# Performance work log

Hardware: AMD Instinct MI355X
Metric: run time of the kernel (lower is better)

Reference implementation:

```python
import jax, jax.numpy as jnp
import numpy as np

N_NODES = 50000
N_EDGES = 400000
D_NODE = 256
D_EDGE = 64
LN_EPS = 1e-6  # flax LayerNorm default


def _layer_norm(x, scale, bias):
    mu = jnp.mean(x, axis=-1, keepdims=True)
    var = jnp.mean(jnp.square(x - mu), axis=-1, keepdims=True)
    return (x - mu) * jax.lax.rsqrt(var + LN_EPS) * scale + bias


def _glorot(key, shape):
    fan_in, fan_out = shape
    std = jnp.sqrt(2.0 / (fan_in + fan_out))
    return std * jax.random.normal(key, shape, dtype=jnp.float32)


def setup_inputs() -> dict:
    key = jax.random.key(0)
    ks = jax.random.split(key, 10)
    inp = {
        "nodes": jax.random.normal(ks[0], (N_NODES, D_NODE), dtype=jnp.float32),
        "edges": jax.random.normal(ks[1], (N_EDGES, D_EDGE), dtype=jnp.float32),
        "senders": jax.random.randint(ks[2], (N_EDGES,), 0, N_NODES, dtype=jnp.int32),
        "receivers": jax.random.randint(ks[3], (N_EDGES,), 0, N_NODES, dtype=jnp.int32),
        # message projection (no bias)
        "W_message": _glorot(ks[4], (D_NODE + D_EDGE, D_NODE)),
        # NodeMLP (ReluMLP_skip) with n_features_list_nodes = [256, 256, 256]
        "mlp_W0": _glorot(ks[5], (D_NODE, D_NODE)), "mlp_b0": jnp.zeros((D_NODE,), jnp.float32),
        "mlp_W1": _glorot(ks[6], (D_NODE, D_NODE)), "mlp_b1": jnp.zeros((D_NODE,), jnp.float32),
        "mlp_W2": _glorot(ks[7], (D_NODE, D_NODE)), "mlp_b2": jnp.zeros((D_NODE,), jnp.float32),
        # LayerNorm params
        "ln_aggr_scale": jnp.ones((D_NODE,), jnp.float32), "ln_aggr_bias": jnp.zeros((D_NODE,), jnp.float32),
        "ln_out_scale": jnp.ones((D_NODE,), jnp.float32), "ln_out_bias": jnp.zeros((D_NODE,), jnp.float32),
    }
    return inp


def _relu_mlp_skip(x, Ws, bs):
    # Dense layers; ReLU on all but the last; residual add whenever widths match.
    n = len(Ws)
    for i, (W, b) in enumerate(zip(Ws, bs)):
        y = x @ W + b
        if i < n - 1:
            y = jax.nn.relu(y)
        x = x + y if y.shape[-1] == x.shape[-1] else y
    return x


def reference(nodes, edges, senders, receivers, W_message,
              mlp_W0, mlp_b0, mlp_W1, mlp_b1, mlp_W2, mlp_b2,
              ln_aggr_scale, ln_aggr_bias, ln_out_scale, ln_out_bias):
    total_nodes = nodes.shape[0]
    sender_features = nodes[senders]                      # [E, d] gather
    msg_in = jnp.concatenate([sender_features, edges], axis=-1)  # [E, d+d_e]
    messages = msg_in @ W_message                          # [E, d]
    agg = jax.ops.segment_sum(messages, receivers, num_segments=total_nodes)  # [N, d]
    h = _layer_norm(jax.nn.relu(agg) + nodes, ln_aggr_scale, ln_aggr_bias)
    nodes_out = _relu_mlp_skip(h, [mlp_W0, mlp_W1, mlp_W2], [mlp_b0, mlp_b1, mlp_b2])
    nodes_new = _layer_norm(nodes + nodes_out, ln_out_scale, ln_out_bias)
    return nodes_new
```

## Files before the change

### kernel.cpp

```cpp
#include <hip/hip_runtime.h>

#define NN 50000
#define NE 400000

typedef unsigned short u16;
typedef unsigned int   u32;
typedef __bf16 bf16x4 __attribute__((ext_vector_type(4)));
typedef __bf16 bf16x8 __attribute__((ext_vector_type(8)));
typedef float  f32x4  __attribute__((ext_vector_type(4)));

union ABFrag { bf16x8 v; bf16x4 h[2]; };
union BFrag  { uint4 u; bf16x8 v; };

__device__ __forceinline__ u16 f2bfu(float f) {
  u32 u = __builtin_bit_cast(u32, f);
  return (u16)((u + 0x7FFFu + ((u >> 16) & 1u)) >> 16);
}
__device__ __forceinline__ float bf2f(u16 u) {
  return __builtin_bit_cast(float, (u32)u << 16);
}

__device__ __forceinline__ void pack_one(const float* __restrict__ W,
                                         u16* __restrict__ P, int idx) {
  int k = idx >> 8, n = idx & 255;
  int t = k >> 5, kp = k & 31;
  int g = (kp & 15) >> 2;
  int j = (kp & 3) | ((kp >> 4) << 2);
  P[(((t << 8) + n) << 5) + (g << 3) + j] = f2bfu(W[idx]);
}

#define NB_CVT  12500
#define NB_PACK 1088
#define NB_HIST 1563

__global__ __launch_bounds__(256) void k_prep(
    const float* __restrict__ nodes, u16* __restrict__ nodes_bf,
    const float* __restrict__ Wm, const float* __restrict__ W0,
    const float* __restrict__ W1, const float* __restrict__ W2,
    u16* __restrict__ Pm, u16* __restrict__ P0,
    u16* __restrict__ P1, u16* __restrict__ P2,
    const int* __restrict__ recv, int* __restrict__ cnt)
{
  int b = blockIdx.x, t = threadIdx.x;
  if (b < NB_CVT) {
    int i = b * 256 + t;
    float4 f = ((const float4*)nodes)[i];
    ushort4 o;
    o.x = f2bfu(f.x); o.y = f2bfu(f.y); o.z = f2bfu(f.z); o.w = f2bfu(f.w);
    ((ushort4*)nodes_bf)[i] = o;
  } else if (b < NB_CVT + NB_PACK) {
    int idx = (b - NB_CVT) * 256 + t;
    const int S0 = 320 * 256, S1 = S0 + 65536, S2 = S1 + 65536;
    if (idx < S0)      pack_one(Wm, Pm, idx);
    else if (idx < S1) pack_one(W0, P0, idx - S0);
    else if (idx < S2) pack_one(W1, P1, idx - S1);
    else               pack_one(W2, P2, idx - S2);
  } else {
    int i = (b - NB_CVT - NB_PACK) * 256 + t;
    if (i < NE) atomicAdd(&cnt[recv[i]], 1);
  }
}

__global__ __launch_bounds__(256) void k_scan1(const int* __restrict__ cnt,
                                               int* __restrict__ loc,
                                               int* __restrict__ bsum) {
  __shared__ int sm[256];
  int t = threadIdx.x, i = blockIdx.x * 256 + t;
  int v = (i < NN) ? cnt[i] : 0;
  sm[t] = v;
  __syncthreads();
  #pragma unroll
  for (int d = 1; d < 256; d <<= 1) {
    int x = sm[t];
    int y = (t >= d) ? sm[t - d] : 0;
    __syncthreads();
    sm[t] = x + y;
    __syncthreads();
  }
  if (i < NN) loc[i] = sm[t] - v;
  if (t == 255) bsum[blockIdx.x] = sm[255];
}

__global__ __launch_bounds__(256) void k_scan2(int* __restrict__ bsum,
                                               int* __restrict__ bpre, int nb) {
  __shared__ int sm[256];
  int t = threadIdx.x;
  int v = (t < nb) ? bsum[t] : 0;
  sm[t] = v;
  __syncthreads();
  #pragma unroll
  for (int d = 1; d < 256; d <<= 1) {
    int x = sm[t];
    int y = (t >= d) ? sm[t - d] : 0;
    __syncthreads();
    sm[t] = x + y;
    __syncthreads();
  }
  if (t < nb) bpre[t] = sm[t] - v;
}

__global__ __launch_bounds__(256) void k_scan3(const int* __restrict__ loc,
                                               const int* __restrict__ bpre,
                                               int* __restrict__ offs,
                                               int* __restrict__ cursor) {
  int i = blockIdx.x * 256 + threadIdx.x;
  if (i < NN) {
    int o = loc[i] + bpre[blockIdx.x];
    offs[i] = o;
    cursor[i] = o;
  }
  if (i == NN - 1) offs[NN] = NE;
}

__global__ __launch_bounds__(256) void k_scatter(
    const int* __restrict__ snd, const int* __restrict__ recv,
    int* __restrict__ cursor, int2* __restrict__ s_pair) {
  int e = blockIdx.x * 256 + threadIdx.x;
  if (e < NE) {
    int p = atomicAdd(&cursor[recv[e]], 1);
    int2 pr; pr.x = snd[e]; pr.y = e;
    s_pair[p] = pr;
  }
}

__global__ __launch_bounds__(256) void k_aggr(
    const u16* __restrict__ nodes_bf, const float* __restrict__ edges,
    const int* __restrict__ offs, const int2* __restrict__ s_pair,
    u16* __restrict__ X)
{
  const int node = blockIdx.x * 4 + (threadIdx.x >> 6);
  const int lane = threadIdx.x & 63;
  const int h = lane >> 5, c = lane & 31;
  const int beg = offs[node], end = offs[node + 1];

  float a0 = 0.f, a1 = 0.f, a2 = 0.f, a3 = 0.f;
  float a4 = 0.f, a5 = 0.f, a6 = 0.f, a7 = 0.f;
  float ae0 = 0.f, ae1 = 0.f;

  for (int jb = beg; jb < end; jb += 8) {
    int j = jb + (lane & 7);
    if (j >= end) j = end - 1;
    int2 pr = s_pair[j];
    const int rem = end - jb;

#define PGATHER(K) \
    int s##K = __shfl(pr.x, 2 * K + h); \
    int e##K = __shfl(pr.y, 2 * K + h); \
    uint4 n##K = *(const uint4*)(nodes_bf + (size_t)s##K * 256 + (c << 3)); \
    float2 v##K = *(const float2*)(edges + (size_t)e##K * 64 + (c << 1));

    PGATHER(0) PGATHER(1) PGATHER(2) PGATHER(3)
#undef PGATHER

#define PACC(K) \
    if (rem > 2 * K + h) { \
      a0 += bf2f((u16)n##K.x); a1 += bf2f((u16)(n##K.x >> 16)); \
      a2 += bf2f((u16)n##K.y); a3 += bf2f((u16)(n##K.y >> 16)); \
      a4 += bf2f((u16)n##K.z); a5 += bf2f((u16)(n##K.z >> 16)); \
      a6 += bf2f((u16)n##K.w); a7 += bf2f((u16)(n##K.w >> 16)); \
      ae0 += v##K.x; ae1 += v##K.y; }

    PACC(0) PACC(1) PACC(2) PACC(3)
#undef PACC
  }

  a0 += __shfl_xor(a0, 32); a1 += __shfl_xor(a1, 32);
  a2 += __shfl_xor(a2, 32); a3 += __shfl_xor(a3, 32);
  a4 += __shfl_xor(a4, 32); a5 += __shfl_xor(a5, 32);
  a6 += __shfl_xor(a6, 32); a7 += __shfl_xor(a7, 32);
  ae0 += __shfl_xor(ae0, 32); ae1 += __shfl_xor(ae1, 32);

  if (lane < 32) {
    u16* xr = X + (size_t)node * 320;
    uint4 o;
    o.x = (u32)f2bfu(a0) | ((u32)f2bfu(a1) << 16);
    o.y = (u32)f2bfu(a2) | ((u32)f2bfu(a3) << 16);
    o.z = (u32)f2bfu(a4) | ((u32)f2bfu(a5) << 16);
    o.w = (u32)f2bfu(a6) | ((u32)f2bfu(a7) << 16);
    *(uint4*)(xr + (c << 3)) = o;
    *(u32*)(xr + 256 + (c << 1)) =
        (u32)f2bfu(ae0) | ((u32)f2bfu(ae1) << 16);
  }
}

#define AT_ADDR(r, c) (atb + ((((r) * 640) + ((c) * 2)) ^ (((r) & 7) << 4)))

#define WRBT(c, v) do { int _c = (c); \
  int _i = (((_c >> 10) << 13) + ((_c & 3) << 11) + (((_c & 1023) >> 2) << 3)) ^ ((_c & 3) << 4); \
  *(uint4*)&Bt[_i] = (v); } while (0)

#define MFMA_STEP(t) \
  _Pragma("unroll") \
  for (int kk = 0; kk < 2; ++kk) { \
    ABFrag a; \
    const int kc = (((t) * 2 + kk) << 5) + (g << 2); \
    const int m = wr16 + l16; \
    a.h[0] = *(const bf16x4*)AT_ADDR(m, kc); \
    a.h[1] = *(const bf16x4*)AT_ADDR(m, kc + 16); \
    _Pragma("unroll") \
    for (int q = 0; q < 4; ++q) { \
      BFrag b; \
      b.u = *(const uint4*)&Bt[((kk << 13) + (g << 11) + ((wcn + (q << 4) + l16) << 3)) ^ (g << 4)]; \
      acc[q] = __builtin_amdgcn_mfma_f32_16x16x32_bf16(a.v, b.v, acc[q], 0, 0, 0); \
    } \
  }

#define RUN_LAYER(wp, T) do { \
  const u16* pb = (wp) + ((size_t)tid << 3); \
  uint4 p0 = *(const uint4*)(pb); \
  uint4 p1 = *(const uint4*)(pb + 8192); \
  _Pragma("unroll 1") \
  for (int t = 0; t < (T); ++t) { \
    __syncthreads(); \
    WRBT(tid, p0); WRBT(tid + 1024, p1); \
    if (t + 1 < (T)) { \
      const u16* nb = pb + ((size_t)(t + 1) << 14); \
      p0 = *(const uint4*)nb; p1 = *(const uint4*)(nb + 8192); \
    } \
    __syncthreads(); \
    MFMA_STEP(t) \
  } \
} while (0)

#define LN_STATS() do { \
  _Pragma("unroll") \
  for (int r = 0; r < 4; ++r) { \
    float s  = acc[0][r] + acc[1][r] + acc[2][r] + acc[3][r]; \
    float s2 = acc[0][r]*acc[0][r] + acc[1][r]*acc[1][r] + acc[2][r]*acc[2][r] + acc[3][r]*acc[3][r]; \
    s  += __shfl_xor(s, 1);  s  += __shfl_xor(s, 2);  s  += __shfl_xor(s, 4);  s  += __shfl_xor(s, 8); \
    s2 += __shfl_xor(s2, 1); s2 += __shfl_xor(s2, 2); s2 += __shfl_xor(s2, 4); s2 += __shfl_xor(s2, 8); \
    if (l16 == 0) { int m = wr16 + g4 + r; red[m][wc2] = s; red[m][wc2 + 1] = s2; } \
  } \
  __syncthreads(); \
  if (tid < 64) { \
    float s  = red[tid][0] + red[tid][2] + red[tid][4] + red[tid][6]; \
    float s2 = red[tid][1] + red[tid][3] + red[tid][5] + red[tid][7]; \
    float mu  = s * (1.f / 256.f); \
    float var = s2 * (1.f / 256.f) - mu * mu; \
    murs[tid][0] = mu; murs[tid][1] = rsqrtf(var + 1e-6f); \
  } \
  __syncthreads(); \
} while (0)

__global__ __launch_bounds__(1024)
void k_fused(
    const u16* __restrict__ X, const float* __restrict__ nodes,
    const u16* __restrict__ wm, const u16* __restrict__ w0,
    const u16* __restrict__ w1, const u16* __restrict__ w2,
    const float* __restrict__ b0, const float* __restrict__ b1,
    const float* __restrict__ b2,
    const float* __restrict__ lnAs, const float* __restrict__ lnAb,
    const float* __restrict__ lnOs, const float* __restrict__ lnOb,
    float* __restrict__ out)
{
  __shared__ u16 At[64 * 320];
  __shared__ u16 Bt[16384];
  __shared__ float red[64][8];
  __shared__ float murs[64][2];

  const int tid = threadIdx.x;
  const int lane = tid & 63;
  const int w16 = tid >> 6;
  const int wr16 = (w16 >> 2) << 4;
  const int wcn = (w16 & 3) << 6;
  const int wc2 = (w16 & 3) << 1;
  const int l16 = lane & 15, g = lane >> 4, g4 = g << 2;
  const int r0 = blockIdx.x * 64;

  char* const atb = (char*)At;

  #pragma unroll
  for (int it = 0; it < 3; ++it) {
    int c = tid + it * 1024;
    if (c < 2560) {
      int r = c / 40, seg = c - r * 40;
      int row = r0 + r;
      uint4 v = {0u, 0u, 0u, 0u};
      if (row < NN) v = *(const uint4*)(X + (size_t)row * 320 + seg * 8);
      *(uint4*)(atb + ((r * 640 + seg * 16) ^ ((r & 7) << 4))) = v;
    }
  }

  f32x4 acc[4];
  const f32x4 z = {0.f, 0.f, 0.f, 0.f};
  #pragma unroll
  for (int q = 0; q < 4; ++q) acc[q] = z;

  RUN_LAYER(wm, 5);

  #pragma unroll
  for (int q = 0; q < 4; ++q) {
    int n = wcn + (q << 4) + l16;
    #pragma unroll
    for (int r = 0; r < 4; ++r) {
      int row = r0 + wr16 + g4 + r;
      float nv = (row < NN) ? nodes[(size_t)row * 256 + n] : 0.f;
      acc[q][r] = fmaxf(acc[q][r], 0.f) + nv;
    }
  }
  LN_STATS();
  #pragma unroll
  for (int q = 0; q < 4; ++q) {
    int n = wcn + (q << 4) + l16;
    float scl = lnAs[n], bia = lnAb[n];
    #pragma unroll
    for (int r = 0; r < 4; ++r) {
      int m = wr16 + g4 + r;
      float h = (acc[q][r] - murs[m][0]) * murs[m][1] * scl + bia;
      *(u16*)AT_ADDR(m, n) = f2bfu(h);
      acc[q][r] = 0.f;
    }
  }

  #pragma unroll 1
  for (int l = 0; l < 3; ++l) {
    const u16* wp = (l == 0) ? w0 : (l == 1) ? w1 : w2;
    RUN_LAYER(wp, 4);
    __syncthreads();

    if (l < 2) {
      const float* bp = (l == 0) ? b0 : b1;
      #pragma unroll
      for (int q = 0; q < 4; ++q) {
        int n = wcn + (q << 4) + l16;
        float bn = bp[n];
        #pragma unroll
        for (int r = 0; r < 4; ++r) {
          int m = wr16 + g4 + r;
          u16* p = (u16*)AT_ADDR(m, n);
          float xn = bf2f(*p) + fmaxf(acc[q][r] + bn, 0.f);
          *p = f2bfu(xn);
          acc[q][r] = 0.f;
        }
      }
    } else {
      #pragma unroll
      for (int q = 0; q < 4; ++q) {
        int n = wcn + (q << 4) + l16;
        float bn = b2[n];
        #pragma unroll
        for (int r = 0; r < 4; ++r) {
          int m = wr16 + g4 + r;
          int row = r0 + m;
          float nv = (row < NN) ? nodes[(size_t)row * 256 + n] : 0.f;
          acc[q][r] = nv + bf2f(*(const u16*)AT_ADDR(m, n)) + acc[q][r] + bn;
        }
      }
    }
  }

  LN_STATS();
  #pragma unroll
  for (int q = 0; q < 4; ++q) {
    int n = wcn + (q << 4) + l16;
    float scl = lnOs[n], bia = lnOb[n];
    #pragma unroll
    for (int r = 0; r < 4; ++r) {
      int m = wr16 + g4 + r;
      int row = r0 + m;
      if (row < NN)
        out[(size_t)row * 256 + n] =
            (acc[q][r] - murs[m][0]) * murs[m][1] * scl + bia;
    }
  }
}

extern "C" void kernel_launch(void* const* d_in, const int* in_sizes, int n_in,
                              void* d_out, int out_size, void* d_ws, size_t ws_size,
                              hipStream_t stream)
{
  const float* nodes = (const float*)d_in[0];
  const float* edges = (const float*)d_in[1];
  const int* senders = (const int*)d_in[2];
  const int* receivers = (const int*)d_in[3];
  const float* Wmsg = (const float*)d_in[4];
  const float* W0 = (const float*)d_in[5];
  const float* b0 = (const float*)d_in[6];
  const float* W1 = (const float*)d_in[7];
  const float* b1 = (const float*)d_in[8];
  const float* W2 = (const float*)d_in[9];
  const float* b2 = (const float*)d_in[10];
  const float* lnAs = (const float*)d_in[11];
  const float* lnAb = (const float*)d_in[12];
  const float* lnOs = (const float*)d_in[13];
  const float* lnOb = (const float*)d_in[14];
  float* out = (float*)d_out;
  (void)in_sizes; (void)n_in; (void)out_size; (void)ws_size;

  char* w = (char*)d_ws;
  size_t off = 0;
  auto take = [&](size_t b) { void* p = w + off; off += (b + 511) & ~(size_t)511; return p; };

  u16*   nodes_bf = (u16*)take((size_t)NN * 256 * 2);
  u16*   wmsg_p   = (u16*)take(320 * 256 * 2);
  u16*   w0_p     = (u16*)take(256 * 256 * 2);
  u16*   w1_p     = (u16*)take(256 * 256 * 2);
  u16*   w2_p     = (u16*)take(256 * 256 * 2);
  u16*   X        = (u16*)take((size_t)NN * 320 * 2);
  int*   cnt      = (int*)take((size_t)NN * 4);
  int*   loc      = (int*)take((size_t)NN * 4);
  int*   offs     = (int*)take((size_t)(NN + 1) * 4);
  int*   cursor   = (int*)take((size_t)NN * 4);
  int2*  s_pair   = (int2*)take((size_t)NE * 8);
  int*   bsum     = (int*)take(256 * 4);
  int*   bpre     = (int*)take(256 * 4);

  const int NB = (NN + 255) / 256;

  hipMemsetAsync(cnt, 0, (size_t)NN * 4, stream);
  k_prep<<<NB_CVT + NB_PACK + NB_HIST, 256, 0, stream>>>(
      nodes, nodes_bf, Wmsg, W0, W1, W2, wmsg_p, w0_p, w1_p, w2_p,
      receivers, cnt);

  k_scan1<<<NB, 256, 0, stream>>>(cnt, loc, bsum);
  k_scan2<<<1, 256, 0, stream>>>(bsum, bpre, NB);
  k_scan3<<<NB, 256, 0, stream>>>(loc, bpre, offs, cursor);
  k_scatter<<<(NE + 255) / 256, 256, 0, stream>>>(senders, receivers, cursor, s_pair);

  k_aggr<<<NN / 4, 256, 0, stream>>>(nodes_bf, edges, offs, s_pair, X);

  const int MB = (NN + 63) / 64;
  k_fused<<<MB, 1024, 0, stream>>>(X, nodes, wmsg_p, w0_p, w1_p, w2_p,
                                   b0, b1, b2, lnAs, lnAb, lnOs, lnOb, out);
}
```

Measured before the change: 219.9 us.

## Switch fused node MLP to 32x32x16 MFMA with 512-thread blocks

Rewrites the fused message/MLP/LayerNorm kernel to use 32x32x16 bf16 MFMA instructions instead of 16x16x32, with each wave owning a 32x64 output tile in two 16-element accumulators. The weight packing layout and LDS B-tile staging change to K-steps of 16 with a halved shared buffer, and the block shrinks from 1024 to 512 threads. The aim is fewer LDS fragment loads per FLOP and better MFMA throughput. The cost is more K-loop iterations with a barrier each, plus higher register pressure from 32 accumulator registers per thread.

Measured after the change: 245.1 us. 11.4% more time.

```diff
diff --git a/kernel.cpp b/kernel.cpp
--- a/kernel.cpp
+++ b/kernel.cpp
@@ -7,7 +7,7 @@
 typedef unsigned int   u32;
 typedef __bf16 bf16x4 __attribute__((ext_vector_type(4)));
 typedef __bf16 bf16x8 __attribute__((ext_vector_type(8)));
-typedef float  f32x4  __attribute__((ext_vector_type(4)));
+typedef float  f32x16 __attribute__((ext_vector_type(16)));
 
 union ABFrag { bf16x8 v; bf16x4 h[2]; };
 union BFrag  { uint4 u; bf16x8 v; };
@@ -23,10 +23,10 @@
 __device__ __forceinline__ void pack_one(const float* __restrict__ W,
                                          u16* __restrict__ P, int idx) {
   int k = idx >> 8, n = idx & 255;
-  int t = k >> 5, kp = k & 31;
-  int g = (kp & 15) >> 2;
-  int j = (kp & 3) | ((kp >> 4) << 2);
-  P[(((t << 8) + n) << 5) + (g << 3) + j] = f2bfu(W[idx]);
+  int t16 = k >> 4, kp = k & 15;
+  int hh = (kp >> 2) & 1;
+  int j = (kp & 3) | (((kp >> 3) & 1) << 2);
+  P[(((t16 << 8) + n) << 4) + (hh << 3) + j] = f2bfu(W[idx]);
 }
 
 #define NB_CVT  12500
@@ -183,53 +183,57 @@
   }
 }
 
+
 #define AT_ADDR(r, c) (atb + ((((r) * 640) + ((c) * 2)) ^ (((r) & 7) << 4)))
 
-#define WRBT(c, v) do { int _c = (c); \
-  int _i = (((_c >> 10) << 13) + ((_c & 3) << 11) + (((_c & 1023) >> 2) << 3)) ^ ((_c & 3) << 4); \
-  *(uint4*)&Bt[_i] = (v); } while (0)
-
-#define MFMA_STEP(t) \
+#define WRBT32(c, v) do { int _c = (c); \
+  *(uint4*)&Bt[((_c >> 9) << 12) + ((_c & 1) << 11) + (((_c >> 1) & 255) << 3)] = (v); \
+} while (0)
+
+#define MFMA_STEP32(t) \
   _Pragma("unroll") \
-  for (int kk = 0; kk < 2; ++kk) { \
+  for (int s = 0; s < 2; ++s) { \
     ABFrag a; \
-    const int kc = (((t) * 2 + kk) << 5) + (g << 2); \
-    const int m = wr16 + l16; \
-    a.h[0] = *(const bf16x4*)AT_ADDR(m, kc); \
-    a.h[1] = *(const bf16x4*)AT_ADDR(m, kc + 16); \
-    _Pragma("unroll") \
-    for (int q = 0; q < 4; ++q) { \
-      BFrag b; \
-      b.u = *(const uint4*)&Bt[((kk << 13) + (g << 11) + ((wcn + (q << 4) + l16) << 3)) ^ (g << 4)]; \
-      acc[q] = __builtin_amdgcn_mfma_f32_16x16x32_bf16(a.v, b.v, acc[q], 0, 0, 0); \
-    } \
-  }
-
-#define RUN_LAYER(wp, T) do { \
+    const int kc = ((t) << 5) + (s << 4) + (h << 2); \
+    a.h[0] = *(const bf16x4*)AT_ADDR(mrow, kc); \
+    a.h[1] = *(const bf16x4*)AT_ADDR(mrow, kc + 8); \
+    const int bi = (s << 12) + (h << 11) + ((wcn + m32) << 3); \
+    BFrag bA, bB; \
+    bA.u = *(const uint4*)&Bt[bi]; \
+    bB.u = *(const uint4*)&Bt[bi + 256]; \
+    accA = __builtin_amdgcn_mfma_f32_32x32x16_bf16(a.v, bA.v, accA, 0, 0, 0); \
+    accB = __builtin_amdgcn_mfma_f32_32x32x16_bf16(a.v, bB.v, accB, 0, 0, 0); \
+  }
+
+#define RUN_LAYER32(wp, T) do { \
   const u16* pb = (wp) + ((size_t)tid << 3); \
   uint4 p0 = *(const uint4*)(pb); \
-  uint4 p1 = *(const uint4*)(pb + 8192); \
+  uint4 p1 = *(const uint4*)(pb + 4096); \
   _Pragma("unroll 1") \
   for (int t = 0; t < (T); ++t) { \
     __syncthreads(); \
-    WRBT(tid, p0); WRBT(tid + 1024, p1); \
+    WRBT32(tid, p0); WRBT32(tid + 512, p1); \
     if (t + 1 < (T)) { \
-      const u16* nb = pb + ((size_t)(t + 1) << 14); \
-      p0 = *(const uint4*)nb; p1 = *(const uint4*)(nb + 8192); \
+      const u16* nb = pb + ((size_t)(t + 1) << 13); \
+      p0 = *(const uint4*)nb; p1 = *(const uint4*)(nb + 4096); \
     } \
     __syncthreads(); \
-    MFMA_STEP(t) \
+    MFMA_STEP32(t) \
   } \
 } while (0)
 
-#define LN_STATS() do { \
+#define ROW_OF(rg) (((rg) & 3) + (((rg) >> 2) << 3) + (h << 2))
+
+#define LN_STATS32() do { \
   _Pragma("unroll") \
-  for (int r = 0; r < 4; ++r) { \
-    float s  = acc[0][r] + acc[1][r] + acc[2][r] + acc[3][r]; \
-    float s2 = acc[0][r]*acc[0][r] + acc[1][r]*acc[1][r] + acc[2][r]*acc[2][r] + acc[3][r]*acc[3][r]; \
-    s  += __shfl_xor(s, 1);  s  += __shfl_xor(s, 2);  s  += __shfl_xor(s, 4);  s  += __shfl_xor(s, 8); \
-    s2 += __shfl_xor(s2, 1); s2 += __shfl_xor(s2, 2); s2 += __shfl_xor(s2, 4); s2 += __shfl_xor(s2, 8); \
-    if (l16 == 0) { int m = wr16 + g4 + r; red[m][wc2] = s; red[m][wc2 + 1] = s2; } \
+  for (int rg = 0; rg < 16; ++rg) { \
+    float va = accA[rg], vb = accB[rg]; \
+    float s = va + vb, s2 = va * va + vb * vb; \
+    s  += __shfl_xor(s, 1);  s  += __shfl_xor(s, 2);  s  += __shfl_xor(s, 4); \
+    s  += __shfl_xor(s, 8);  s  += __shfl_xor(s, 16); \
+    s2 += __shfl_xor(s2, 1); s2 += __shfl_xor(s2, 2); s2 += __shfl_xor(s2, 4); \
+    s2 += __shfl_xor(s2, 8); s2 += __shfl_xor(s2, 16); \
+    if (m32 == 0) { int mm = wr32 + ROW_OF(rg); red[mm][wc2] = s; red[mm][wc2 + 1] = s2; } \
   } \
   __syncthreads(); \
   if (tid < 64) { \
@@ -242,7 +246,7 @@
   __syncthreads(); \
 } while (0)
 
-__global__ __launch_bounds__(1024)
+__global__ __launch_bounds__(512)
 void k_fused(
     const u16* __restrict__ X, const float* __restrict__ nodes,
     const u16* __restrict__ wm, const u16* __restrict__ w0,
@@ -254,113 +258,115 @@
     float* __restrict__ out)
 {
   __shared__ u16 At[64 * 320];
-  __shared__ u16 Bt[16384];
+  __shared__ u16 Bt[8192];
   __shared__ float red[64][8];
   __shared__ float murs[64][2];
 
   const int tid = threadIdx.x;
   const int lane = tid & 63;
-  const int w16 = tid >> 6;
-  const int wr16 = (w16 >> 2) << 4;
-  const int wcn = (w16 & 3) << 6;
-  const int wc2 = (w16 & 3) << 1;
-  const int l16 = lane & 15, g = lane >> 4, g4 = g << 2;
+  const int w = tid >> 6;
+  const int wr32 = (w >> 2) << 5;
+  const int wcn = (w & 3) << 6;
+  const int wc2 = (w & 3) << 1;
+  const int m32 = lane & 31, h = lane >> 5;
+  const int mrow = wr32 + m32;
   const int r0 = blockIdx.x * 64;
 
   char* const atb = (char*)At;
 
   #pragma unroll
-  for (int it = 0; it < 3; ++it) {
-    int c = tid + it * 1024;
-    if (c < 2560) {
-      int r = c / 40, seg = c - r * 40;
-      int row = r0 + r;
-      uint4 v = {0u, 0u, 0u, 0u};
-      if (row < NN) v = *(const uint4*)(X + (size_t)row * 320 + seg * 8);
-      *(uint4*)(atb + ((r * 640 + seg * 16) ^ ((r & 7) << 4))) = v;
+  for (int it = 0; it < 5; ++it) {
+    int c = tid + it * 512;
+    int r = c / 40, seg = c - r * 40;
+    int row = r0 + r;
+    uint4 v = {0u, 0u, 0u, 0u};
+    if (row < NN) v = *(const uint4*)(X + (size_t)row * 320 + seg * 8);
+    *(uint4*)(atb + ((r * 640 + seg * 16) ^ ((r & 7) << 4))) = v;
+  }
+
+  f32x16 accA, accB;
+  #pragma unroll
+  for (int i = 0; i < 16; ++i) { accA[i] = 0.f; accB[i] = 0.f; }
+
+  RUN_LAYER32(wm, 10);
+
+  #pragma unroll
+  for (int rg = 0; rg < 16; ++rg) {
+    int row = r0 + wr32 + ROW_OF(rg);
+    float nA = 0.f, nB = 0.f;
+    if (row < NN) {
+      nA = nodes[(size_t)row * 256 + wcn + m32];
+      nB = nodes[(size_t)row * 256 + wcn + 32 + m32];
     }
-  }
-
-  f32x4 acc[4];
-  const f32x4 z = {0.f, 0.f, 0.f, 0.f};
-  #pragma unroll
-  for (int q = 0; q < 4; ++q) acc[q] = z;
-
-  RUN_LAYER(wm, 5);
-
-  #pragma unroll
-  for (int q = 0; q < 4; ++q) {
-    int n = wcn + (q << 4) + l16;
+    accA[rg] = fmaxf(accA[rg], 0.f) + nA;
+    accB[rg] = fmaxf(accB[rg], 0.f) + nB;
+  }
+  LN_STATS32();
+  {
+    float sclA = lnAs[wcn + m32], biaA = lnAb[wcn + m32];
+    float sclB = lnAs[wcn + 32 + m32], biaB = lnAb[wcn + 32 + m32];
     #pragma unroll
-    for (int r = 0; r < 4; ++r) {
-      int row = r0 + wr16 + g4 + r;
-      float nv = (row < NN) ? nodes[(size_t)row * 256 + n] : 0.f;
-      acc[q][r] = fmaxf(acc[q][r], 0.f) + nv;
-    }
-  }
-  LN_STATS();
-  #pragma unroll
-  for (int q = 0; q < 4; ++q) {
-    int n = wcn + (q << 4) + l16;
-    float scl = lnAs[n], bia = lnAb[n];
-    #pragma unroll
-    for (int r = 0; r < 4; ++r) {
-      int m = wr16 + g4 + r;
-      float h = (acc[q][r] - murs[m][0]) * murs[m][1] * scl + bia;
-      *(u16*)AT_ADDR(m, n) = f2bfu(h);
-      acc[q][r] = 0.f;
+    for (int rg = 0; rg < 16; ++rg) {
+      int mm = wr32 + ROW_OF(rg);
+      float mu = murs[mm][0], rs = murs[mm][1];
+      float hA = (accA[rg] - mu) * rs * sclA + biaA;
+      float hB = (accB[rg] - mu) * rs * sclB + biaB;
+      *(u16*)AT_ADDR(mm, wcn + m32) = f2bfu(hA);
+      *(u16*)AT_ADDR(mm, wcn + 32 + m32) = f2bfu(hB);
+      accA[rg] = 0.f; accB[rg] = 0.f;
     }
   }
 
   #pragma unroll 1
   for (int l = 0; l < 3; ++l) {
     const u16* wp = (l == 0) ? w0 : (l == 1) ? w1 : w2;
-    RUN_LAYER(wp, 4);
+    RUN_LAYER32(wp, 8);
     __syncthreads();
 
     if (l < 2) {
       const float* bp = (l == 0) ? b0 : b1;
+      float bnA = bp[wcn + m32], bnB = bp[wcn + 32 + m32];
       #pragma unroll
-      for (int q = 0; q < 4; ++q) {
-        int n = wcn + (q << 4) + l16;
-        float bn = bp[n];
-        #pragma unroll
-        for (int r = 0; r < 4; ++r) {
-          int m = wr16 + g4 + r;
-          u16* p = (u16*)AT_ADDR(m, n);
-          float xn = bf2f(*p) + fmaxf(acc[q][r] + bn, 0.f);
-          *p = f2bfu(xn);
-          acc[q][r] = 0.f;
-        }
+      for (int rg = 0; rg < 16; ++rg) {
+        int mm = wr32 + ROW_OF(rg);
+        u16* pA = (u16*)AT_ADDR(mm, wcn + m32);
+        u16* pB = (u16*)AT_ADDR(mm, wcn + 32 + m32);
+        float xA = bf2f(*pA) + fmaxf(accA[rg] + bnA, 0.f);
+        float xB = bf2f(*pB) + fmaxf(accB[rg] + bnB, 0.f);
+        *pA = f2bfu(xA);
+        *pB = f2bfu(xB);
+        accA[rg] = 0.f; accB[rg] = 0.f;
       }
     } else {
+      float bnA = b2[wcn + m32], bnB = b2[wcn + 32 + m32];
       #pragma unroll
-      for (int q = 0; q < 4; ++q) {
-        int n = wcn + (q << 4) + l16;
-        float bn = b2[n];
-        #pragma unroll
-        for (int r = 0; r < 4; ++r) {
-          int m = wr16 + g4 + r;
-          int row = r0 + m;
-          float nv = (row < NN) ? nodes[(size_t)row * 256 + n] : 0.f;
-          acc[q][r] = nv + bf2f(*(const u16*)AT_ADDR(m, n)) + acc[q][r] + bn;
+      for (int rg = 0; rg < 16; ++rg) {
+        int mm = wr32 + ROW_OF(rg);
+        int row = r0 + mm;
+        float nA = 0.f, nB = 0.f;
+        if (row < NN) {
+          nA = nodes[(size_t)row * 256 + wcn + m32];
+          nB = nodes[(size_t)row * 256 + wcn + 32 + m32];
         }
+        accA[rg] = nA + bf2f(*(const u16*)AT_ADDR(mm, wcn + m32)) + accA[rg] + bnA;
+        accB[rg] = nB + bf2f(*(const u16*)AT_ADDR(mm, wcn + 32 + m32)) + accB[rg] + bnB;
       }
     }
   }
 
-  LN_STATS();
-  #pragma unroll
-  for (int q = 0; q < 4; ++q) {
-    int n = wcn + (q << 4) + l16;
-    float scl = lnOs[n], bia = lnOb[n];
+  LN_STATS32();
+  {
+    float sclA = lnOs[wcn + m32], biaA = lnOb[wcn + m32];
+    float sclB = lnOs[wcn + 32 + m32], biaB = lnOb[wcn + 32 + m32];
     #pragma unroll
-    for (int r = 0; r < 4; ++r) {
-      int m = wr16 + g4 + r;
-      int row = r0 + m;
-      if (row < NN)
-        out[(size_t)row * 256 + n] =
-            (acc[q][r] - murs[m][0]) * murs[m][1] * scl + bia;
+    for (int rg = 0; rg < 16; ++rg) {
+      int mm = wr32 + ROW_OF(rg);
+      int row = r0 + mm;
+      if (row < NN) {
+        float mu = murs[mm][0], rs = murs[mm][1];
+        out[(size_t)row * 256 + wcn + m32] = (accA[rg] - mu) * rs * sclA + biaA;
+        out[(size_t)row * 256 + wcn + 32 + m32] = (accB[rg] - mu) * rs * sclB + biaB;
+      }
     }
   }
 }
@@ -420,6 +426,6 @@
   k_aggr<<<NN / 4, 256, 0, stream>>>(nodes_bf, edges, offs, s_pair, X);
 
   const int MB = (NN + 63) / 64;
-  k_fused<<<MB, 1024, 0, stream>>>(X, nodes, wmsg_p, w0_p, w1_p, w2_p,
-                                   b0, b1, b2, lnAs, lnAb, lnOs, lnOb, out);
-}
+  k_fused<<<MB, 512, 0, stream>>>(X, nodes, wmsg_p, w0_p, w1_p, w2_p,
+                                  b0, b1, b2, lnAs, lnAb, lnOs, lnOb, out);
+}
```
